# Performance work log

Measured on AMD Instinct MI355X. Metric: run time of the kernel, lower is better.

Reference implementation:

```python
import jax, jax.numpy as jnp
import numpy as np

N = 100_000   # nodes
C = 32        # classes
E = 3_200_000 # edges


def setup_inputs() -> dict:
    key = jax.random.key(0)
    k1, k2, k3, k4, k5 = jax.random.split(key, 5)
    edge_index = jax.random.randint(k1, (2, E), 0, N, dtype=jnp.int32)
    edge_weight = jax.random.uniform(k2, (E,), dtype=jnp.float32) + 0.1  # positive weights
    inputs = jax.random.normal(k3, (N, C), dtype=jnp.float32)
    labels = jax.random.randint(k4, (N,), 0, C)
    y = jax.nn.one_hot(labels, C, dtype=jnp.float32)  # torch.where(y[:, i]) implies one-hot labels
    sample_mask = jax.random.bernoulli(k5, 0.5, (N,))
    return {"edge_index": edge_index, "edge_weight": edge_weight,
            "inputs": inputs, "y": y, "sample_mask": sample_mask}


def _normalize_sparse(edge_index, edge_weight, n):
    # normalize_sparse_tensor: add self-loops (weight 1), then D^{-1/2} A D^{-1/2}
    loop = jnp.arange(n, dtype=edge_index.dtype)
    row = jnp.concatenate([edge_index[0], loop])
    col = jnp.concatenate([edge_index[1], loop])
    w = jnp.concatenate([edge_weight, jnp.ones((n,), edge_weight.dtype)])
    deg = jax.ops.segment_sum(w, row, num_segments=n)
    dinv = jnp.where(deg > 0, jax.lax.rsqrt(deg), 0.0)
    vals = dinv[row] * w * dinv[col]
    return row, col, vals


def reference(edge_index, edge_weight, inputs, y, sample_mask):
    n, c = inputs.shape
    row, col, vals = _normalize_sparse(edge_index, edge_weight, n)

    p = jax.nn.softmax(inputs, axis=1)
    m = sample_mask.astype(p.dtype)[:, None]
    p = p * (1.0 - m) + y * m          # replace predictions by labels on masked nodes
    ym = y * m                          # labels only on masked nodes

    # nodeH = raw_normed_adj @ p   (sparse spmm)  -> (n, c)
    nodeH = jax.ops.segment_sum(vals[:, None] * p[col], row, num_segments=n)

    # per-class mean of nodeH over nodes with label i (one-hot => sum/count)
    cnt = ym.sum(axis=0)                         # (c,)
    H = (ym.T @ nodeH) / cnt[:, None]            # (c, c); NaN rows if class empty

    # NaN fixups (identity when no NaNs present)
    Hn = jnp.isnan(H)
    H = jnp.where(Hn, H.T, H)
    Hn = jnp.isnan(H)
    H0 = jnp.where(Hn, jnp.zeros_like(H), H)
    miss = (1.0 - H0.sum(axis=1, keepdims=True)) / Hn.sum(axis=1, keepdims=True).astype(H.dtype)
    H = jnp.where(Hn, miss, H0)

    # makeDoubleStochasticH: iterate col-norm then row-norm; 'delta' = ||H||_1 (as in source)
    def cond(state):
        _, i, d = state
        return (d >= 1e-12) & (i < 3000)

    def body(state):
        Hc, i, _ = state
        Hc = Hc / Hc.sum(axis=0, keepdims=True)
        Hc = Hc / Hc.sum(axis=1, keepdims=True)
        return Hc, i + 1, jnp.abs(Hc).sum()

    H, _, _ = jax.lax.while_loop(cond, body, (H, jnp.int32(0), jnp.float32(1e30)))
    return H
```

## Files before the change

kernel.cpp:

```cpp
#include <hip/hip_runtime.h>
#include <hip/hip_fp16.h>


#define RS 40960
#define BDEG 85
#define W 200
#define NBKTMAX 512
#define BCAP 4608
#define LCAP 4096
#define NSC 512
#define NPR NBKTMAX
#define NTOT (1 + NPR)
#define NRED 16
#define RPER ((NTOT + NRED - 1) / NRED)
#define PPAD 204
#define BVW 3200
#define L2A (BVW / 2)

__global__ __launch_bounds__(1024) void
k_deg(const int* __restrict__ ei, const float* __restrict__ ew,
      __half* __restrict__ slab, const unsigned char* __restrict__ mask_bytes,
      int* __restrict__ flag, float* __restrict__ Hg, float* __restrict__ cnt,
      int* __restrict__ gCnt, int E_, int R) {
  __shared__ float h[RS];
  if (blockIdx.x == 0) {
    Hg[threadIdx.x] = 0.f;
    if (threadIdx.x < 32) cnt[threadIdx.x] = 0.f;
    if (threadIdx.x < NBKTMAX) gCnt[threadIdx.x] = 0;
    int* hi = (int*)h;
    if (threadIdx.x == 0) hi[0] = 0;
    __syncthreads();
    int acc = mask_bytes[threadIdx.x * 4 + 1] | mask_bytes[threadIdx.x * 4 + 2]
            | mask_bytes[threadIdx.x * 4 + 3];
    if (acc) atomicOr(&hi[0], 1);
    __syncthreads();
    if (threadIdx.x == 0) *flag = (hi[0] != 0) ? 1 : 0;
  }
  int r = blockIdx.x % R;
  int sl = blockIdx.x / R;
  for (int i = threadIdx.x; i < RS; i += 1024) h[i] = 0.f;
  __syncthreads();
  int lo = r * RS;
  int Q = E_ >> 2;
  int q0 = (int)((long long)Q * sl / BDEG);
  int q1 = (int)((long long)Q * (sl + 1) / BDEG);
  const int4* ei4 = (const int4*)ei;
  const float4* ew4 = (const float4*)ew;
  int q = q0 + threadIdx.x;
  for (; q + 1024 < q1; q += 2048) {
    int4 ia = ei4[q], ib = ei4[q + 1024];
    float4 wa = ew4[q], wb = ew4[q + 1024];
    unsigned o0 = (unsigned)(ia.x - lo), o1 = (unsigned)(ia.y - lo);
    unsigned o2 = (unsigned)(ia.z - lo), o3 = (unsigned)(ia.w - lo);
    unsigned o4 = (unsigned)(ib.x - lo), o5 = (unsigned)(ib.y - lo);
    unsigned o6 = (unsigned)(ib.z - lo), o7 = (unsigned)(ib.w - lo);
    if (o0 < RS) atomicAdd(&h[o0], wa.x);
    if (o1 < RS) atomicAdd(&h[o1], wa.y);
    if (o2 < RS) atomicAdd(&h[o2], wa.z);
    if (o3 < RS) atomicAdd(&h[o3], wa.w);
    if (o4 < RS) atomicAdd(&h[o4], wb.x);
    if (o5 < RS) atomicAdd(&h[o5], wb.y);
    if (o6 < RS) atomicAdd(&h[o6], wb.z);
    if (o7 < RS) atomicAdd(&h[o7], wb.w);
  }
  for (; q < q1; q += 1024) {
    int4 idx = ei4[q];
    float4 w = ew4[q];
    unsigned o0 = (unsigned)(idx.x - lo), o1 = (unsigned)(idx.y - lo);
    unsigned o2 = (unsigned)(idx.z - lo), o3 = (unsigned)(idx.w - lo);
    if (o0 < RS) atomicAdd(&h[o0], w.x);
    if (o1 < RS) atomicAdd(&h[o1], w.y);
    if (o2 < RS) atomicAdd(&h[o2], w.z);
    if (o3 < RS) atomicAdd(&h[o3], w.w);
  }
  if (sl == BDEG - 1) {
    for (int e = (Q << 2) + threadIdx.x; e < E_; e += 1024) {
      unsigned off = (unsigned)(ei[e] - lo);
      if (off < RS) atomicAdd(&h[off], ew[e]);
    }
  }
  __syncthreads();
  __half* dst = slab + ((size_t)r * BDEG + sl) * RS;
  for (int i = threadIdx.x; i < RS; i += 1024) dst[i] = __float2half(h[i]);
}

__global__ void k_node(const float* __restrict__ x, const float* __restrict__ y,
                       const void* __restrict__ maskp, const int* __restrict__ flag,
                       const __half* __restrict__ slab, int2* __restrict__ ninfo,
                       __half* __restrict__ p16, float* __restrict__ Hg,
                       float* __restrict__ cnt, unsigned* __restrict__ bitvec, int Nn) {
  __shared__ float scnt[32], sdiag[32];
  if (threadIdx.x < 32) { scnt[threadIdx.x] = 0.f; sdiag[threadIdx.x] = 0.f; }
  __syncthreads();
  int n = blockIdx.x * blockDim.x + threadIdx.x;
  bool inb = (n < Nn);
  bool byteMask = (*flag != 0);
  bool msk = false;
  if (inb)
    msk = byteMask ? (((const unsigned char*)maskp)[n] != 0)
                   : (((const int*)maskp)[n] != 0);
  unsigned long long bm = __ballot(msk);
  if ((threadIdx.x & 63) == 0)
    ((unsigned long long*)bitvec)[n >> 6] = bm;
  if (inb) {
    const __half* sl = slab + ((size_t)(n / RS) * BDEG) * RS + (n % RS);
    float d = 0.f;
    #pragma unroll 5
    for (int bb = 0; bb < BDEG; ++bb) d += __half2float(sl[(size_t)bb * RS]);
    float dinv = rsqrtf(d + 1.0f);
    int a = -1;
    if (msk) {
      const float4* yi = (const float4*)(y + (size_t)n * 32);
      #pragma unroll
      for (int q = 0; q < 8; ++q) {
        float4 v = yi[q];
        if (v.x == 1.f) a = q * 4 + 0;
        if (v.y == 1.f) a = q * 4 + 1;
        if (v.z == 1.f) a = q * 4 + 2;
        if (v.w == 1.f) a = q * 4 + 3;
      }
      atomicAdd(&scnt[a], 1.f);
      atomicAdd(&sdiag[a], dinv * dinv);
    } else {
      const float4* xi = (const float4*)(x + (size_t)n * 32);
      float xs[32];
      #pragma unroll
      for (int q = 0; q < 8; ++q) {
        float4 v = xi[q];
        xs[q*4+0] = v.x; xs[q*4+1] = v.y; xs[q*4+2] = v.z; xs[q*4+3] = v.w;
      }
      float mx = -3.4e38f;
      #pragma unroll
      for (int i = 0; i < 32; ++i) mx = fmaxf(mx, xs[i]);
      float s = 0.f;
      #pragma unroll
      for (int i = 0; i < 32; ++i) { xs[i] = __expf(xs[i] - mx); s += xs[i]; }
      float inv = 1.f / s;
      union { short sh[32]; int4 v[4]; } u;
      #pragma unroll
      for (int i = 0; i < 32; ++i)
        u.sh[i] = __half_as_short(__float2half(xs[i] * inv));
      int4* po = (int4*)(p16 + (size_t)n * 32);
      #pragma unroll
      for (int q = 0; q < 4; ++q) po[q] = u.v[q];
    }
    int2 ni; ni.x = __float_as_int(dinv); ni.y = a;
    ninfo[n] = ni;
  }
  __syncthreads();
  if (threadIdx.x < 32) {
    if (scnt[threadIdx.x] != 0.f) atomicAdd(&cnt[threadIdx.x], scnt[threadIdx.x]);
    if (sdiag[threadIdx.x] != 0.f) atomicAdd(&Hg[threadIdx.x * 33], sdiag[threadIdx.x]);
  }
}

__global__ __launch_bounds__(1024) void
k_bucket(const int* __restrict__ ei, const float* __restrict__ ew,
         const int2* __restrict__ ninfo, const unsigned* __restrict__ bitvec,
         int2* __restrict__ gBucket, int* __restrict__ gCnt, int E_) {
  __shared__ int2 list[LCAP];
  __shared__ int lcnt;
  __shared__ int bcnt[NBKTMAX];
  __shared__ int gbase[NBKTMAX];
  __shared__ int bplace[NBKTMAX];
  __shared__ int sbase[NBKTMAX];
  union USH { unsigned sbv[BVW]; int2 l2[L2A]; };
  __shared__ USH us;
  __shared__ int2 l2b[LCAP - L2A];
  if (threadIdx.x == 0) lcnt = 0;
  if (threadIdx.x < NBKTMAX) { bcnt[threadIdx.x] = 0; bplace[threadIdx.x] = 0; }
  for (int i = threadIdx.x; i < BVW; i += 1024) us.sbv[i] = bitvec[i];
  __syncthreads();
  int E4 = E_ >> 2;
  int q0 = (int)((long long)E4 * blockIdx.x / NSC);
  int q1 = (int)((long long)E4 * (blockIdx.x + 1) / NSC);
  for (int q = q0 + threadIdx.x; q < q1; q += 1024) {
    int4 rr = ((const int4*)ei)[q];
    int4 cc = ((const int4*)(ei + E_))[q];
    float4 ww = ((const float4*)ew)[q];
    int rs[4] = {rr.x, rr.y, rr.z, rr.w};
    int cs[4] = {cc.x, cc.y, cc.z, cc.w};
    float wv[4] = {ww.x, ww.y, ww.z, ww.w};
    bool act[4];
    #pragma unroll
    for (int k = 0; k < 4; ++k)
      act[k] = (us.sbv[(unsigned)rs[k] >> 5] >> (rs[k] & 31)) & 1;
    int2 nr[4];
    #pragma unroll
    for (int k = 0; k < 4; ++k)
      if (act[k]) nr[k] = ninfo[rs[k]];
    #pragma unroll
    for (int k = 0; k < 4; ++k) {
      if (act[k]) {
        float val = __int_as_float(nr[k].x) * wv[k];
        int pos = atomicAdd(&lcnt, 1);
        if (pos < LCAP) list[pos] = make_int2((cs[k] << 5) | nr[k].y, __float_as_int(val));
      }
    }
  }
  if (blockIdx.x == NSC - 1) {
    for (int e = (E4 << 2) + threadIdx.x; e < E_; e += 1024) {
      int r = ei[e];
      if (!((us.sbv[(unsigned)r >> 5] >> (r & 31)) & 1)) continue;
      int2 nr = ninfo[r];
      int c = ei[E_ + e];
      float val = __int_as_float(nr.x) * ew[e];
      int pos = atomicAdd(&lcnt, 1);
      if (pos < LCAP) list[pos] = make_int2((c << 5) | nr.y, __float_as_int(val));
    }
  }
  __syncthreads();
  int nl = min(lcnt, LCAP);
  for (int i = threadIdx.x; i < nl; i += 1024)
    atomicAdd(&bcnt[(list[i].x >> 5) / W], 1);
  __syncthreads();
  if (threadIdx.x < NBKTMAX) sbase[threadIdx.x] = bcnt[threadIdx.x];
  __syncthreads();
  for (int off = 1; off < NBKTMAX; off <<= 1) {
    int v = 0;
    if (threadIdx.x < NBKTMAX && threadIdx.x >= off) v = sbase[threadIdx.x - off];
    __syncthreads();
    if (threadIdx.x < NBKTMAX && threadIdx.x >= off) sbase[threadIdx.x] += v;
    __syncthreads();
  }
  if (threadIdx.x < NBKTMAX) {
    int n = bcnt[threadIdx.x];
    gbase[threadIdx.x] = (n > 0) ? atomicAdd(&gCnt[threadIdx.x], n) : 0;
  }
  __syncthreads();
  for (int i = threadIdx.x; i < nl; i += 1024) {
    int2 rec = list[i];
    int bkt = (rec.x >> 5) / W;
    int d = sbase[bkt] - bcnt[bkt] + atomicAdd(&bplace[bkt], 1);
    if (d < L2A) us.l2[d] = rec; else l2b[d - L2A] = rec;
  }
  __syncthreads();
  for (int j = threadIdx.x; j < nl; j += 1024) {
    int2 rec = (j < L2A) ? us.l2[j] : l2b[j - L2A];
    int bkt = (rec.x >> 5) / W;
    int dst = gbase[bkt] + (j - (sbase[bkt] - bcnt[bkt]));
    if (dst < BCAP) gBucket[(size_t)bkt * BCAP + dst] = rec;
  }
}

__global__ __launch_bounds__(1024) void
k_process(const int2* __restrict__ gBucket, const int* __restrict__ gCnt,
          const int2* __restrict__ ninfo, const __half* __restrict__ p16,
          float* __restrict__ procSlab, int Nn) {
  __shared__ float TlocT[32 * W];
  __shared__ __half plocT[32 * PPAD];
  __shared__ float H32[1024];
  __shared__ float ldin[W];
  __shared__ int   llab[W];
  int k = blockIdx.x;
  int c0 = k * W;
  int Wb = min(c0 + W, Nn) - c0;
  for (int i = threadIdx.x; i < 32 * W; i += 1024) TlocT[i] = 0.f;
  H32[threadIdx.x] = 0.f;
  if ((int)threadIdx.x < Wb) {
    int2 ni = ninfo[c0 + threadIdx.x];
    ldin[threadIdx.x] = __int_as_float(ni.x);
    llab[threadIdx.x] = ni.y;
  }
  __syncthreads();
  if (Wb > 0) {
    for (int i = threadIdx.x; i < Wb * 32; i += 1024) {
      int c = i >> 5, b = i & 31;
      plocT[b * PPAD + c] = p16[(size_t)(c0 + c) * 32 + b];
    }
    int n = min(gCnt[k], BCAP);
    const int2* bk = gBucket + (size_t)k * BCAP;
    for (int i = threadIdx.x; i < n; i += 1024) {
      int2 rec = bk[i];
      int cl = (rec.x >> 5) - c0;
      int a = rec.x & 31;
      float v = __int_as_float(rec.y) * ldin[cl];
      int b = llab[cl];
      if (b >= 0) atomicAdd(&H32[a * 32 + b], v);
      else        atomicAdd(&TlocT[a * W + cl], v);
    }
  }
  __syncthreads();
  int a = threadIdx.x >> 5;
  int b = threadIdx.x & 31;
  float acc0 = 0.f, acc1 = 0.f, acc2 = 0.f, acc3 = 0.f;
  int c = 0;
  for (; c + 3 < Wb; c += 4) {
    float4 tv = *(const float4*)&TlocT[a * W + c];
    short4 ps = *(const short4*)&plocT[b * PPAD + c];
    acc0 += tv.x * __half2float(__short_as_half(ps.x));
    acc1 += tv.y * __half2float(__short_as_half(ps.y));
    acc2 += tv.z * __half2float(__short_as_half(ps.z));
    acc3 += tv.w * __half2float(__short_as_half(ps.w));
  }
  for (; c < Wb; ++c)
    acc0 += TlocT[a * W + c] * __half2float(plocT[b * PPAD + c]);
  procSlab[(size_t)k * 1024 + threadIdx.x] =
      (acc0 + acc1) + (acc2 + acc3) + H32[threadIdx.x];
}

__global__ __launch_bounds__(1024) void
k_red(const float* __restrict__ allSlabs, float* __restrict__ red) {
  int k0 = blockIdx.x * RPER;
  int k1 = min(k0 + RPER, NTOT);
  float s = 0.f;
  for (int k = k0; k < k1; ++k) s += allSlabs[(size_t)k * 1024 + threadIdx.x];
  red[(size_t)blockIdx.x * 1024 + threadIdx.x] = s;
}

__global__ __launch_bounds__(1024) void
k_sinkhorn(const float* __restrict__ red, const float* __restrict__ cnt,
           float* __restrict__ out) {
  __shared__ float sHH[1024];
  int t = threadIdx.x;
  float s = 0.f;
  #pragma unroll
  for (int k = 0; k < NRED; ++k) s += red[(size_t)k * 1024 + t];
  sHH[t] = s;
  __syncthreads();
  int j = t;
  if (j >= 32) return;
  float cj = cnt[j];
  float Hcol[32], Hrow[32];
  #pragma unroll
  for (int i = 0; i < 32; ++i) Hcol[i] = sHH[i * 32 + j];
  #pragma unroll
  for (int i = 0; i < 32; ++i) Hcol[i] /= __shfl(cj, i);
  #pragma unroll
  for (int k = 0; k < 32; ++k) Hrow[k] = sHH[j * 32 + k] / cj;
  float u = 1.f, v = 1.f;
  for (int it = 0; it < 40; ++it) {
    float a0 = 0.f, a1 = 0.f, a2 = 0.f, a3 = 0.f;
    #pragma unroll
    for (int i = 0; i < 32; i += 4) {
      a0 += Hcol[i+0] * __shfl(u, i+0);
      a1 += Hcol[i+1] * __shfl(u, i+1);
      a2 += Hcol[i+2] * __shfl(u, i+2);
      a3 += Hcol[i+3] * __shfl(u, i+3);
    }
    v = 1.f / ((a0 + a1) + (a2 + a3));
    a0 = a1 = a2 = a3 = 0.f;
    #pragma unroll
    for (int k = 0; k < 32; k += 4) {
      a0 += Hrow[k+0] * __shfl(v, k+0);
      a1 += Hrow[k+1] * __shfl(v, k+1);
      a2 += Hrow[k+2] * __shfl(v, k+2);
      a3 += Hrow[k+3] * __shfl(v, k+3);
    }
    u = 1.f / ((a0 + a1) + (a2 + a3));
  }
  #pragma unroll
  for (int i = 0; i < 32; ++i) out[i * 32 + j] = __shfl(u, i) * Hcol[i] * v;
}

extern "C" void kernel_launch(void* const* d_in, const int* in_sizes, int n_in,
                              void* d_out, int out_size, void* d_ws, size_t ws_size,
                              hipStream_t stream) {
  const int*   ei   = (const int*)d_in[0];
  const float* ew   = (const float*)d_in[1];
  const float* x    = (const float*)d_in[2];
  const float* y    = (const float*)d_in[3];
  const void*  mask = d_in[4];
  float* out = (float*)d_out;
  int E_ = in_sizes[1];
  int Nn = in_sizes[2] / 32;
  int R = (Nn + RS - 1) / RS;

  char* ws = (char*)d_ws;
  size_t o = 0;
  float* cnt = (float*)(ws + o);    o += 128;
  int*   flag = (int*)(ws + o);     o += 128;
  int*   gCnt = (int*)(ws + o);     o += NBKTMAX * 4;
  float* allSlabs = (float*)(ws + o);
  float* Hg       = allSlabs;
  float* procSlab = allSlabs + 1024;
  o += (size_t)NTOT * 4096;
  float* red = (float*)(ws + o);    o += (size_t)NRED * 4096;
  int2*  gBucket = (int2*)(ws + o); o += (size_t)NBKTMAX * BCAP * 8;
  __half* slab = (__half*)(ws + o); o += (size_t)R * BDEG * RS * 2;
  int2*  ninfo = (int2*)(ws + o);   o += (size_t)Nn * 8;
  __half* p16 = (__half*)(ws + o);  o += (size_t)Nn * 64;
  unsigned* gbv = (unsigned*)(ws + o); o += (size_t)BVW * 4;

  int nb = (Nn + 255) / 256;
  k_deg<<<R * BDEG, 1024, 0, stream>>>(ei, ew, slab, (const unsigned char*)mask,
                                       flag, Hg, cnt, gCnt, E_, R);
  k_node<<<nb, 256, 0, stream>>>(x, y, mask, flag, slab, ninfo, p16, Hg, cnt, gbv, Nn);
  k_bucket<<<NSC, 1024, 0, stream>>>(ei, ew, ninfo, gbv, gBucket, gCnt, E_);
  k_process<<<NPR, 1024, 0, stream>>>(gBucket, gCnt, ninfo, p16, procSlab, Nn);
  k_red<<<NRED, 1024, 0, stream>>>(allSlabs, red);
  k_sinkhorn<<<1, 1024, 0, stream>>>(red, cnt, out);
}
```

Measured before the change: 218.8 us.

## Replace LDS-slab degree histogram with direct global float atomics

The degree computation no longer builds per-range shared-memory histograms written out as fp16 slabs that k_node then sums over 85 slices. Instead it zeroes a per-node float degree array with a memset and has 512 blocks scatter global atomicAdds straight into it, so k_node reads a single value per node. This removes the slab write and the 85-way strided reduction, and each block now reads its share of the edges once rather than the same edges being scanned for every node range. In exchange it relies on contended global atomics over a 100k-entry array, and the order of float additions becomes nondeterministic.

```diff
diff --git a/kernel.cpp b/kernel.cpp
--- a/kernel.cpp
+++ b/kernel.cpp
@@ -2,8 +2,6 @@
 #include <hip/hip_fp16.h>
 
 
-#define RS 40960
-#define BDEG 85
 #define W 200
 #define NBKTMAX 512
 #define BCAP 4608
@@ -19,74 +17,44 @@
 
 __global__ __launch_bounds__(1024) void
 k_deg(const int* __restrict__ ei, const float* __restrict__ ew,
-      __half* __restrict__ slab, const unsigned char* __restrict__ mask_bytes,
+      float* __restrict__ deg, const unsigned char* __restrict__ mask_bytes,
       int* __restrict__ flag, float* __restrict__ Hg, float* __restrict__ cnt,
-      int* __restrict__ gCnt, int E_, int R) {
-  __shared__ float h[RS];
+      int* __restrict__ gCnt, int E_) {
   if (blockIdx.x == 0) {
     Hg[threadIdx.x] = 0.f;
     if (threadIdx.x < 32) cnt[threadIdx.x] = 0.f;
     if (threadIdx.x < NBKTMAX) gCnt[threadIdx.x] = 0;
-    int* hi = (int*)h;
-    if (threadIdx.x == 0) hi[0] = 0;
+    __shared__ int shi;
+    if (threadIdx.x == 0) shi = 0;
     __syncthreads();
     int acc = mask_bytes[threadIdx.x * 4 + 1] | mask_bytes[threadIdx.x * 4 + 2]
             | mask_bytes[threadIdx.x * 4 + 3];
-    if (acc) atomicOr(&hi[0], 1);
+    if (acc) atomicOr(&shi, 1);
     __syncthreads();
-    if (threadIdx.x == 0) *flag = (hi[0] != 0) ? 1 : 0;
-  }
-  int r = blockIdx.x % R;
-  int sl = blockIdx.x / R;
-  for (int i = threadIdx.x; i < RS; i += 1024) h[i] = 0.f;
-  __syncthreads();
-  int lo = r * RS;
+    if (threadIdx.x == 0) *flag = (shi != 0) ? 1 : 0;
+  }
   int Q = E_ >> 2;
-  int q0 = (int)((long long)Q * sl / BDEG);
-  int q1 = (int)((long long)Q * (sl + 1) / BDEG);
   const int4* ei4 = (const int4*)ei;
   const float4* ew4 = (const float4*)ew;
-  int q = q0 + threadIdx.x;
-  for (; q + 1024 < q1; q += 2048) {
-    int4 ia = ei4[q], ib = ei4[q + 1024];
-    float4 wa = ew4[q], wb = ew4[q + 1024];
-    unsigned o0 = (unsigned)(ia.x - lo), o1 = (unsigned)(ia.y - lo);
-    unsigned o2 = (unsigned)(ia.z - lo), o3 = (unsigned)(ia.w - lo);
-    unsigned o4 = (unsigned)(ib.x - lo), o5 = (unsigned)(ib.y - lo);
-    unsigned o6 = (unsigned)(ib.z - lo), o7 = (unsigned)(ib.w - lo);
-    if (o0 < RS) atomicAdd(&h[o0], wa.x);
-    if (o1 < RS) atomicAdd(&h[o1], wa.y);
-    if (o2 < RS) atomicAdd(&h[o2], wa.z);
-    if (o3 < RS) atomicAdd(&h[o3], wa.w);
-    if (o4 < RS) atomicAdd(&h[o4], wb.x);
-    if (o5 < RS) atomicAdd(&h[o5], wb.y);
-    if (o6 < RS) atomicAdd(&h[o6], wb.z);
-    if (o7 < RS) atomicAdd(&h[o7], wb.w);
-  }
-  for (; q < q1; q += 1024) {
+  int q0 = (int)((long long)Q * blockIdx.x / NSC);
+  int q1 = (int)((long long)Q * (blockIdx.x + 1) / NSC);
+  for (int q = q0 + threadIdx.x; q < q1; q += 1024) {
     int4 idx = ei4[q];
     float4 w = ew4[q];
-    unsigned o0 = (unsigned)(idx.x - lo), o1 = (unsigned)(idx.y - lo);
-    unsigned o2 = (unsigned)(idx.z - lo), o3 = (unsigned)(idx.w - lo);
-    if (o0 < RS) atomicAdd(&h[o0], w.x);
-    if (o1 < RS) atomicAdd(&h[o1], w.y);
-    if (o2 < RS) atomicAdd(&h[o2], w.z);
-    if (o3 < RS) atomicAdd(&h[o3], w.w);
-  }
-  if (sl == BDEG - 1) {
-    for (int e = (Q << 2) + threadIdx.x; e < E_; e += 1024) {
-      unsigned off = (unsigned)(ei[e] - lo);
-      if (off < RS) atomicAdd(&h[off], ew[e]);
-    }
-  }
-  __syncthreads();
-  __half* dst = slab + ((size_t)r * BDEG + sl) * RS;
-  for (int i = threadIdx.x; i < RS; i += 1024) dst[i] = __float2half(h[i]);
+    atomicAdd(&deg[idx.x], w.x);
+    atomicAdd(&deg[idx.y], w.y);
+    atomicAdd(&deg[idx.z], w.z);
+    atomicAdd(&deg[idx.w], w.w);
+  }
+  if (blockIdx.x == NSC - 1) {
+    for (int e = (Q << 2) + threadIdx.x; e < E_; e += 1024)
+      atomicAdd(&deg[ei[e]], ew[e]);
+  }
 }
 
 __global__ void k_node(const float* __restrict__ x, const float* __restrict__ y,
                        const void* __restrict__ maskp, const int* __restrict__ flag,
-                       const __half* __restrict__ slab, int2* __restrict__ ninfo,
+                       const float* __restrict__ deg, int2* __restrict__ ninfo,
                        __half* __restrict__ p16, float* __restrict__ Hg,
                        float* __restrict__ cnt, unsigned* __restrict__ bitvec, int Nn) {
   __shared__ float scnt[32], sdiag[32];
@@ -103,11 +71,7 @@
   if ((threadIdx.x & 63) == 0)
     ((unsigned long long*)bitvec)[n >> 6] = bm;
   if (inb) {
-    const __half* sl = slab + ((size_t)(n / RS) * BDEG) * RS + (n % RS);
-    float d = 0.f;
-    #pragma unroll 5
-    for (int bb = 0; bb < BDEG; ++bb) d += __half2float(sl[(size_t)bb * RS]);
-    float dinv = rsqrtf(d + 1.0f);
+    float dinv = rsqrtf(deg[n] + 1.0f);
     int a = -1;
     if (msk) {
       const float4* yi = (const float4*)(y + (size_t)n * 32);
@@ -364,7 +328,6 @@
   float* out = (float*)d_out;
   int E_ = in_sizes[1];
   int Nn = in_sizes[2] / 32;
-  int R = (Nn + RS - 1) / RS;
 
   char* ws = (char*)d_ws;
   size_t o = 0;
@@ -377,15 +340,16 @@
   o += (size_t)NTOT * 4096;
   float* red = (float*)(ws + o);    o += (size_t)NRED * 4096;
   int2*  gBucket = (int2*)(ws + o); o += (size_t)NBKTMAX * BCAP * 8;
-  __half* slab = (__half*)(ws + o); o += (size_t)R * BDEG * RS * 2;
+  float* deg = (float*)(ws + o);    o += (size_t)Nn * 4;
   int2*  ninfo = (int2*)(ws + o);   o += (size_t)Nn * 8;
   __half* p16 = (__half*)(ws + o);  o += (size_t)Nn * 64;
   unsigned* gbv = (unsigned*)(ws + o); o += (size_t)BVW * 4;
 
   int nb = (Nn + 255) / 256;
-  k_deg<<<R * BDEG, 1024, 0, stream>>>(ei, ew, slab, (const unsigned char*)mask,
-                                       flag, Hg, cnt, gCnt, E_, R);
-  k_node<<<nb, 256, 0, stream>>>(x, y, mask, flag, slab, ninfo, p16, Hg, cnt, gbv, Nn);
+  hipMemsetAsync(deg, 0, (size_t)Nn * 4, stream);
+  k_deg<<<NSC, 1024, 0, stream>>>(ei, ew, deg, (const unsigned char*)mask,
+                                  flag, Hg, cnt, gCnt, E_);
+  k_node<<<nb, 256, 0, stream>>>(x, y, mask, flag, deg, ninfo, p16, Hg, cnt, gbv, Nn);
   k_bucket<<<NSC, 1024, 0, stream>>>(ei, ew, ninfo, gbv, gBucket, gCnt, E_);
   k_process<<<NPR, 1024, 0, stream>>>(gBucket, gCnt, ninfo, p16, procSlab, Nn);
   k_red<<<NRED, 1024, 0, stream>>>(allSlabs, red);
```

Result: slower. 353.2 us (+61.4%).
